# Performance work log

Hardware: AMD Instinct MI355X
Metric: run time of the kernel (lower is better)

## Reference

```python
import jax, jax.numpy as jnp
import numpy as np

EMBED_DIM = 1024
NUM_HEADS = 16
HEAD_DIM = EMBED_DIM // NUM_HEADS
BATCH = 1
SEQ = 4096


def setup_inputs() -> dict:
    key = jax.random.key(0)
    ks = jax.random.split(key, 9)
    s = 1.0 / np.sqrt(EMBED_DIM)
    inp = {
        "x": jax.random.normal(ks[0], (BATCH, SEQ, EMBED_DIM), dtype=jnp.float32),
        "Wq": jax.random.uniform(ks[1], (EMBED_DIM, EMBED_DIM), jnp.float32, -s, s),
        "bq": jax.random.uniform(ks[2], (EMBED_DIM,), jnp.float32, -s, s),
        "Wk": jax.random.uniform(ks[3], (EMBED_DIM, EMBED_DIM), jnp.float32, -s, s),
        "bk": jax.random.uniform(ks[4], (EMBED_DIM,), jnp.float32, -s, s),
        "Wv": jax.random.uniform(ks[5], (EMBED_DIM, EMBED_DIM), jnp.float32, -s, s),
        "bv": jax.random.uniform(ks[6], (EMBED_DIM,), jnp.float32, -s, s),
        "Wo": jax.random.uniform(ks[7], (EMBED_DIM, EMBED_DIM), jnp.float32, -s, s),
        "bo": jax.random.uniform(ks[8], (EMBED_DIM,), jnp.float32, -s, s),
    }
    return inp


def _attention(x, Wq, bq, Wk, bk, Wv, bv, Wo, bo):
    B, S, E = x.shape
    # project and split heads: [B, H, S, D]
    def split_heads(t):
        return t.reshape(B, S, NUM_HEADS, HEAD_DIM).transpose(0, 2, 1, 3)
    q = split_heads(x @ Wq + bq)
    k = split_heads(x @ Wk + bk)
    v = split_heads(x @ Wv + bv)
    scale = 1.0 / np.sqrt(HEAD_DIM).astype(np.float32)
    # scores: [B, H, S, S] (torch code materializes these per query chunk;
    # math is identical computed in one shot)
    scores = jnp.einsum("bhqd,bhkd->bhqk", q, k) * scale
    attn = jax.nn.softmax(scores, axis=-1)  # dropout p=0 -> identity
    out = jnp.einsum("bhqk,bhkd->bhqd", attn, v)
    out = out.transpose(0, 2, 1, 3).reshape(B, S, E)
    return out @ Wo + bo


def reference(x, Wq, bq, Wk, bk, Wv, bv, Wo, bo):
    return _attention(x, Wq, bq, Wk, bk, Wv, bv, Wo, bo)
```

## Files before the change

### kernel.cpp

```cpp
#include <hip/hip_runtime.h>
#include <stdint.h>

typedef __bf16 bf16;
typedef __bf16 bf16x8 __attribute__((ext_vector_type(8)));
typedef float f32x4 __attribute__((ext_vector_type(4)));

#define EMB 1024
#define SEQ 4096
#define NH 16
#define HD 64

__device__ __forceinline__ void glds16(const void* g, void* l) {
    __builtin_amdgcn_global_load_lds(
        (const __attribute__((address_space(1))) uint32_t*)(uintptr_t)g,
        (__attribute__((address_space(3))) uint32_t*)(uintptr_t)l,
        16, 0, 0);
}

__device__ __forceinline__ void transpose_tile(const float* in, bf16* out,
                                               int R, int C, int rbase, int cbase,
                                               bf16* tile ) {
    const int t = threadIdx.x;
#pragma unroll
    for (int p = 0; p < 2; ++p) {
        int idx = t + p * 256;
        int r = idx >> 3;
        int seg = idx & 7;
        const float* src = in + (size_t)(rbase + r) * C + cbase + seg * 8;
        f32x4 a = *(const f32x4*)src;
        f32x4 b = *(const f32x4*)(src + 4);
#pragma unroll
        for (int i = 0; i < 4; ++i) {
            tile[r * 81 + seg * 8 + i]     = (bf16)a[i];
            tile[r * 81 + seg * 8 + 4 + i] = (bf16)b[i];
        }
    }
    __syncthreads();
#pragma unroll
    for (int p = 0; p < 2; ++p) {
        int idx = t + p * 256;
        int r = idx >> 3;
        int seg = idx & 7;
        bf16x8 v;
#pragma unroll
        for (int i = 0; i < 8; ++i) v[i] = tile[(seg * 8 + i) * 81 + r];
        *(bf16x8*)(out + (size_t)(cbase + r) * R + rbase + seg * 8) = v;
    }
}

__global__ __launch_bounds__(256) void prep_k(const float* __restrict__ W0,
                                              const float* __restrict__ W1,
                                              const float* __restrict__ W2,
                                              bf16* __restrict__ o0,
                                              bf16* __restrict__ o1,
                                              bf16* __restrict__ o2,
                                              const float* __restrict__ x,
                                              bf16* __restrict__ xb) {
    __shared__ bf16 tile[64 * 81];
    if (blockIdx.z < 3) {
        const float* in = blockIdx.z == 0 ? W0 : (blockIdx.z == 1 ? W1 : W2);
        bf16* out = blockIdx.z == 0 ? o0 : (blockIdx.z == 1 ? o1 : o2);
        transpose_tile(in, out, EMB, EMB, blockIdx.y * 64, blockIdx.x * 64, tile);
    } else {
        size_t linear = blockIdx.y * 16 + blockIdx.x;
#pragma unroll
        for (int i = 0; i < 4; ++i) {
            size_t base = linear * 16384 + (size_t)i * 4096 + threadIdx.x * 16;
#pragma unroll
            for (int h = 0; h < 2; ++h) {
                f32x4 a = *(const f32x4*)(x + base + h * 8);
                f32x4 b = *(const f32x4*)(x + base + h * 8 + 4);
                bf16x8 v;
#pragma unroll
                for (int j = 0; j < 4; ++j) { v[j] = (bf16)a[j]; v[4 + j] = (bf16)b[j]; }
                *(bf16x8*)(xb + base + h * 8) = v;
            }
        }
    }
}

__global__ __launch_bounds__(256) void transpose_k(const float* __restrict__ in,
                                                   bf16* __restrict__ out,
                                                   int R, int C) {
    __shared__ bf16 tile[64 * 81];
    transpose_tile(in, out, R, C, blockIdx.y * 64, blockIdx.x * 64, tile);
}

template<bool A_BF16, bool FUSED>
__global__ __launch_bounds__(256, 3) void gemm_m97(
    const void* __restrict__ A,
    const bf16* __restrict__ Wt0, const bf16* __restrict__ Wt1,
    const bf16* __restrict__ Wt2,
    const float* __restrict__ b0, const float* __restrict__ b1,
    const float* __restrict__ b2,
    void* __restrict__ out0, void* __restrict__ out1,
    bf16* __restrict__ outVt) {
    constexpr int SMEM_BYTES = A_BF16 ? (FUSED ? 18432 : 16384) : 24576;
    __shared__ __align__(16) uint8_t smem[SMEM_BYTES];
    float* aF = (float*)smem;
    bf16*  aB = (bf16*)smem;
    bf16*  bL = (bf16*)(smem + (A_BF16 ? 8192 : 16384));

    const int t = threadIdx.x;
    const int lane = t & 63;
    const int wave = t >> 6;
    const int l15 = lane & 15;
    const int quad = lane >> 4;
    const int wrow = (wave >> 1) * 64;
    const int wcol = (wave & 1) * 64;
    const int nb = blockIdx.x;
    const int which = FUSED ? (nb >> 3) : 0;
    const int ncol = (FUSED ? (nb & 7) : nb) * 128;
    const int mblock = blockIdx.y * 128;

    const bf16* Wt = FUSED ? (which == 0 ? Wt0 : (which == 1 ? Wt1 : Wt2)) : Wt0;
    const float* bias = FUSED ? (which == 0 ? b0 : (which == 1 ? b1 : b2)) : b0;

    float bv[4];
#pragma unroll
    for (int nt = 0; nt < 4; ++nt) bv[nt] = bias[ncol + wcol + nt * 16 + l15];

    f32x4 acc[4][4];
#pragma unroll
    for (int mt = 0; mt < 4; ++mt)
#pragma unroll
        for (int nt = 0; nt < 4; ++nt) acc[mt][nt] = (f32x4){0.f, 0.f, 0.f, 0.f};

    const int a4row = lane >> 3, a4seg = lane & 7;
    const int b2row = lane >> 2, b2seg = lane & 3;

    for (int k0 = 0; k0 < EMB; k0 += 32) {
        __syncthreads();
        if constexpr (!A_BF16) {
#pragma unroll
            for (int i = 0; i < 4; ++i) {
                int row = i * 32 + wave * 8 + a4row;
                int sg = a4seg ^ (row & 7);
                glds16((const float*)A + (size_t)(mblock + row) * EMB + k0 + sg * 4,
                       smem + i * 4096 + wave * 1024);
            }
        } else {
#pragma unroll
            for (int i = 0; i < 2; ++i) {
                int row = i * 64 + wave * 16 + b2row;
                int sg = b2seg ^ ((row >> 1) & 3);
                glds16((const bf16*)A + (size_t)(mblock + row) * EMB + k0 + sg * 8,
                       smem + i * 4096 + wave * 1024);
            }
        }
#pragma unroll
        for (int i = 0; i < 2; ++i) {
            int row = i * 64 + wave * 16 + b2row;
            int sg = b2seg ^ ((row >> 1) & 3);
            glds16(Wt + (size_t)(ncol + row) * EMB + k0 + sg * 8,
                   (uint8_t*)bL + i * 4096 + wave * 1024);
        }
        __syncthreads();

        bf16x8 af[4], bfr[4];
#pragma unroll
        for (int mt = 0; mt < 4; ++mt) {
            int rl = wrow + mt * 16 + l15;
            if constexpr (!A_BF16) {
                f32x4 lo = *(const f32x4*)(aF + rl * 32 + ((2 * quad)     ^ (rl & 7)) * 4);
                f32x4 hi = *(const f32x4*)(aF + rl * 32 + ((2 * quad + 1) ^ (rl & 7)) * 4);
#pragma unroll
                for (int j = 0; j < 4; ++j) {
                    af[mt][j]     = (bf16)lo[j];
                    af[mt][4 + j] = (bf16)hi[j];
                }
            } else {
                af[mt] = *(const bf16x8*)(aB + rl * 32 + (quad ^ ((rl >> 1) & 3)) * 8);
            }
        }
#pragma unroll
        for (int nt = 0; nt < 4; ++nt) {
            int rl = wcol + nt * 16 + l15;
            bfr[nt] = *(const bf16x8*)(bL + rl * 32 + (quad ^ ((rl >> 1) & 3)) * 8);
        }
#pragma unroll
        for (int mt = 0; mt < 4; ++mt)
#pragma unroll
            for (int nt = 0; nt < 4; ++nt)
                acc[mt][nt] = __builtin_amdgcn_mfma_f32_16x16x32_bf16(
                    af[mt], bfr[nt], acc[mt][nt], 0, 0, 0);
    }

    if (!FUSED || which < 2) {
        void* outp = FUSED ? (which == 0 ? out0 : out1) : out0;
#pragma unroll
        for (int mt = 0; mt < 4; ++mt)
#pragma unroll
            for (int nt = 0; nt < 4; ++nt)
#pragma unroll
                for (int r = 0; r < 4; ++r) {
                    size_t row = mblock + wrow + mt * 16 + quad * 4 + r;
                    size_t col = ncol + wcol + nt * 16 + l15;
                    float v = acc[mt][nt][r] + bv[nt];
                    if constexpr (FUSED) ((bf16*)outp)[row * EMB + col] = (bf16)v;
                    else                 ((float*)outp)[row * EMB + col] = v;
                }
    } else if constexpr (FUSED) {
        __syncthreads();
        bf16* tr = (bf16*)smem + wave * 2304;
#pragma unroll
        for (int ch = 0; ch < 2; ++ch) {
#pragma unroll
            for (int mt = 0; mt < 4; ++mt)
#pragma unroll
                for (int ntl = 0; ntl < 2; ++ntl)
#pragma unroll
                    for (int r = 0; r < 4; ++r) {
                        int d_local = ntl * 16 + l15;
                        int s_local = mt * 16 + quad * 4 + r;
                        int nt = 2 * ch + ntl;
                        tr[d_local * 72 + s_local] = (bf16)(acc[mt][nt][r] + bv[nt]);
                    }
            int d2 = lane & 31, h2 = lane >> 5;
#pragma unroll
            for (int j = 0; j < 4; ++j) {
                bf16x8 v = *(const bf16x8*)(tr + d2 * 72 + h2 * 32 + j * 8);
                *(bf16x8*)(outVt + (size_t)(ncol + wcol + ch * 32 + d2) * SEQ +
                           mblock + wrow + h2 * 32 + j * 8) = v;
            }
        }
    }
}

__global__ __launch_bounds__(256, 2) void attn_k(bf16* __restrict__ QO,
                                                 const bf16* __restrict__ Km,
                                                 const bf16* __restrict__ Vt,
                                                 const float* __restrict__ Wo,
                                                 bf16* __restrict__ wt_o) {
    __shared__ bf16 k_lds[2][64 * 64];
    __shared__ bf16 v_lds[2][64 * 64];
    __shared__ bf16 p_lds[4][2][16][72];

    if (blockIdx.y == NH) {
        bf16* tile = &k_lds[0][0];
#pragma unroll 1
        for (int i = 0; i < 8; ++i) {
            int tid = blockIdx.x * 8 + i;
            int ty = tid >> 4, tx = tid & 15;
            transpose_tile(Wo, wt_o, EMB, EMB, ty * 64, tx * 64, tile);
            __syncthreads();
        }
        return;
    }

    const int t = threadIdx.x;
    const int lane = t & 63;
    const int wave = t >> 6;
    const int l15 = lane & 15;
    const int quad = lane >> 4;
    const int sw = l15 & 7;
    const int h = blockIdx.y;
    const int qbase = blockIdx.x * 128 + wave * 32;
    const float QSCALE = 0.125f * 1.4426950408889634f;

    const int srow = wave * 16 + (lane >> 3);
    const int ssg  = lane & 7;

    bf16x8 qf[2][2];
#pragma unroll
    for (int qt = 0; qt < 2; ++qt)
#pragma unroll
        for (int kk = 0; kk < 2; ++kk) {
            bf16x8 raw = *(const bf16x8*)(QO + (size_t)(qbase + qt * 16 + l15) * EMB +
                                          h * HD + kk * 32 + quad * 8);
#pragma unroll
            for (int j = 0; j < 8; ++j) qf[qt][kk][j] = (bf16)((float)raw[j] * QSCALE);
        }

    f32x4 o_acc[2][4];
#pragma unroll
    for (int qt = 0; qt < 2; ++qt)
#pragma unroll
        for (int c = 0; c < 4; ++c) o_acc[qt][c] = (f32x4){0.f, 0.f, 0.f, 0.f};
    float l_run[2][4] = {{0.f, 0.f, 0.f, 0.f}, {0.f, 0.f, 0.f, 0.f}};

#define STAGE(buf, kbv)                                                               \
    do {                                                                              \
        _Pragma("unroll")                                                             \
        for (int i = 0; i < 2; ++i) {                                                 \
            int rr = srow + i * 8;                                                    \
            int sg = ssg ^ (rr & 7);                                                  \
            glds16(Km + (size_t)((kbv) + rr) * EMB + h * HD + sg * 8,                 \
                   &k_lds[buf][(wave * 16 + i * 8) * 64]);                            \
            glds16(Vt + (size_t)(h * HD + rr) * SEQ + (kbv) + sg * 8,                 \
                   &v_lds[buf][(wave * 16 + i * 8) * 64]);                            \
        }                                                                             \
    } while (0)

#define COMPUTE(buf)                                                                  \
    do {                                                                              \
        f32x4 s[2][4];                                                                \
        _Pragma("unroll")                                                             \
        for (int c = 0; c < 4; ++c) {                                                 \
            int row = c * 16 + l15;                                                   \
            bf16x8 k0 = *(const bf16x8*)&k_lds[buf][row * 64 + ((quad)     ^ sw) * 8];\
            bf16x8 k1 = *(const bf16x8*)&k_lds[buf][row * 64 + ((4 + quad) ^ sw) * 8];\
            _Pragma("unroll")                                                         \
            for (int qt = 0; qt < 2; ++qt) {                                          \
                f32x4 z = (f32x4){0.f, 0.f, 0.f, 0.f};                                \
                z = __builtin_amdgcn_mfma_f32_16x16x32_bf16(qf[qt][0], k0, z, 0, 0, 0);\
                s[qt][c] = __builtin_amdgcn_mfma_f32_16x16x32_bf16(qf[qt][1], k1, z, 0, 0, 0);\
            }                                                                         \
        }                                                                             \
        _Pragma("unroll")                                                             \
        for (int qt = 0; qt < 2; ++qt)                                                \
            _Pragma("unroll")                                                         \
            for (int r = 0; r < 4; ++r)                                               \
                _Pragma("unroll")                                                     \
                for (int c = 0; c < 4; ++c) {                                         \
                    float p = __builtin_amdgcn_exp2f(s[qt][c][r]);                    \
                    l_run[qt][r] += p;                                                \
                    p_lds[wave][qt][quad * 4 + r][c * 16 + l15] = (bf16)p;            \
                }                                                                     \
        bf16x8 pf[2][2];                                                              \
        _Pragma("unroll")                                                             \
        for (int qt = 0; qt < 2; ++qt)                                                \
            _Pragma("unroll")                                                         \
            for (int tt = 0; tt < 2; ++tt)                                            \
                pf[qt][tt] = *(const bf16x8*)&p_lds[wave][qt][l15][tt * 32 + quad * 8];\
        _Pragma("unroll")                                                             \
        for (int c = 0; c < 4; ++c) {                                                 \
            int row = c * 16 + l15;                                                   \
            bf16x8 v0 = *(const bf16x8*)&v_lds[buf][row * 64 + ((quad)     ^ sw) * 8];\
            bf16x8 v1 = *(const bf16x8*)&v_lds[buf][row * 64 + ((4 + quad) ^ sw) * 8];\
            _Pragma("unroll")                                                         \
            for (int qt = 0; qt < 2; ++qt) {                                          \
                o_acc[qt][c] = __builtin_amdgcn_mfma_f32_16x16x32_bf16(               \
                    pf[qt][0], v0, o_acc[qt][c], 0, 0, 0);                            \
                o_acc[qt][c] = __builtin_amdgcn_mfma_f32_16x16x32_bf16(               \
                    pf[qt][1], v1, o_acc[qt][c], 0, 0, 0);                            \
            }                                                                         \
        }                                                                             \
    } while (0)

    STAGE(0, 0);
    for (int kb = 0; kb < SEQ; kb += 128) {
        __syncthreads();
        STAGE(1, kb + 64);
        COMPUTE(0);
        __syncthreads();
        if (kb + 128 < SEQ) STAGE(0, kb + 128);
        COMPUTE(1);
    }
#undef STAGE
#undef COMPUTE

#pragma unroll
    for (int qt = 0; qt < 2; ++qt)
#pragma unroll
        for (int r = 0; r < 4; ++r) {
            float l = l_run[qt][r];
#pragma unroll
            for (int off = 1; off < 16; off <<= 1) l += __shfl_xor(l, off);
            float inv = 1.0f / l;
#pragma unroll
            for (int c = 0; c < 4; ++c)
                QO[(size_t)(qbase + qt * 16 + quad * 4 + r) * EMB + h * HD + c * 16 + l15] =
                    (bf16)(o_acc[qt][c][r] * inv);
        }
}

extern "C" void kernel_launch(void* const* d_in, const int* in_sizes, int n_in,
                              void* d_out, int out_size, void* d_ws, size_t ws_size,
                              hipStream_t stream) {
    const float* x  = (const float*)d_in[0];
    const float* Wq = (const float*)d_in[1];
    const float* bq = (const float*)d_in[2];
    const float* Wk = (const float*)d_in[3];
    const float* bk = (const float*)d_in[4];
    const float* Wv = (const float*)d_in[5];
    const float* bv = (const float*)d_in[6];
    const float* Wo = (const float*)d_in[7];
    const float* bo = (const float*)d_in[8];

    const size_t MAT = (size_t)SEQ * EMB;
    const size_t WMT = (size_t)EMB * EMB;

    bf16* o16   = (bf16*)d_out;
    bf16* Wt_q  = o16;
    bf16* Wt_k  = o16 + WMT;
    bf16* Wt_v  = o16 + 2 * WMT;
    bf16* Vtb   = o16 + 3 * WMT;

    bf16* wsb   = (bf16*)d_ws;
    bf16* QOb   = wsb;
    bf16* Kb    = wsb + MAT;
    bf16* xb    = wsb + 2 * MAT;

    dim3 blk(256);
    dim3 gP(16, 16, 4);
    dim3 gF(24, SEQ / 128);
    dim3 gO(EMB / 128, SEQ / 128);

    if (ws_size >= 3 * MAT * sizeof(bf16)) {
        prep_k<<<gP, blk, 0, stream>>>(Wq, Wk, Wv, Wt_q, Wt_k, Wt_v, x, xb);

        gemm_m97<true, true><<<gF, blk, 0, stream>>>(
            xb, Wt_q, Wt_k, Wt_v, bq, bk, bv, QOb, Kb, Vtb);

        dim3 gA(SEQ / 128, NH + 1);
        attn_k<<<gA, blk, 0, stream>>>(QOb, Kb, Vtb, Wo, xb);

        gemm_m97<true, false><<<gO, blk, 0, stream>>>(
            QOb, xb, nullptr, nullptr, bo, nullptr, nullptr, d_out, nullptr, nullptr);
    } else {
        bf16* Wt_o = wsb + MAT;
        dim3 gTW(EMB / 64, EMB / 64);
        transpose_k<<<gTW, blk, 0, stream>>>(Wq, Wt_q, EMB, EMB);
        transpose_k<<<gTW, blk, 0, stream>>>(Wk, Wt_k, EMB, EMB);
        transpose_k<<<gTW, blk, 0, stream>>>(Wv, Wt_v, EMB, EMB);
        gemm_m97<false, true><<<gF, blk, 0, stream>>>(
            x, Wt_q, Wt_k, Wt_v, bq, bk, bv, QOb, Kb, Vtb);
        dim3 gA(SEQ / 128, NH);
        attn_k<<<gA, blk, 0, stream>>>(QOb, Kb, Vtb, nullptr, nullptr);
        transpose_k<<<gTW, blk, 0, stream>>>(Wo, Wt_o, EMB, EMB);
        gemm_m97<true, false><<<gO, blk, 0, stream>>>(
            QOb, Wt_o, nullptr, nullptr, bo, nullptr, nullptr, d_out, nullptr, nullptr);
    }
}
```

Before: 243.1 us.

## Split attention block into 8 waves of 16 query rows each

The attention kernel now launches 512 threads per block, with each of 8 waves owning 16 query rows instead of 4 waves owning 32. K/V staging is spread over all 8 waves, and the Wo transpose path is templated for 512 threads. The aim is more waves in flight to hide LDS and exp latency, with lower per-wave register pressure. The cost is that each K/V tile loaded into LDS is reused by only one query tile per wave, so there is less MFMA work per LDS read, and barriers now synchronise more waves.

```diff
diff --git a/kernel.cpp b/kernel.cpp
--- a/kernel.cpp
+++ b/kernel.cpp
@@ -17,13 +17,15 @@
         16, 0, 0);
 }
 
+template<int NT>
 __device__ __forceinline__ void transpose_tile(const float* in, bf16* out,
                                                int R, int C, int rbase, int cbase,
                                                bf16* tile ) {
     const int t = threadIdx.x;
-#pragma unroll
-    for (int p = 0; p < 2; ++p) {
-        int idx = t + p * 256;
+    constexpr int PASSES = 512 / NT;
+#pragma unroll
+    for (int p = 0; p < PASSES; ++p) {
+        int idx = t + p * NT;
         int r = idx >> 3;
         int seg = idx & 7;
         const float* src = in + (size_t)(rbase + r) * C + cbase + seg * 8;
@@ -37,8 +39,8 @@
     }
     __syncthreads();
 #pragma unroll
-    for (int p = 0; p < 2; ++p) {
-        int idx = t + p * 256;
+    for (int p = 0; p < PASSES; ++p) {
+        int idx = t + p * NT;
         int r = idx >> 3;
         int seg = idx & 7;
         bf16x8 v;
@@ -60,7 +62,7 @@
     if (blockIdx.z < 3) {
         const float* in = blockIdx.z == 0 ? W0 : (blockIdx.z == 1 ? W1 : W2);
         bf16* out = blockIdx.z == 0 ? o0 : (blockIdx.z == 1 ? o1 : o2);
-        transpose_tile(in, out, EMB, EMB, blockIdx.y * 64, blockIdx.x * 64, tile);
+        transpose_tile<256>(in, out, EMB, EMB, blockIdx.y * 64, blockIdx.x * 64, tile);
     } else {
         size_t linear = blockIdx.y * 16 + blockIdx.x;
 #pragma unroll
@@ -83,7 +85,7 @@
                                                    bf16* __restrict__ out,
                                                    int R, int C) {
     __shared__ bf16 tile[64 * 81];
-    transpose_tile(in, out, R, C, blockIdx.y * 64, blockIdx.x * 64, tile);
+    transpose_tile<256>(in, out, R, C, blockIdx.y * 64, blockIdx.x * 64, tile);
 }
 
 template<bool A_BF16, bool FUSED>
@@ -227,14 +229,14 @@
     }
 }
 
-__global__ __launch_bounds__(256, 2) void attn_k(bf16* __restrict__ QO,
+__global__ __launch_bounds__(512, 4) void attn_k(bf16* __restrict__ QO,
                                                  const bf16* __restrict__ Km,
                                                  const bf16* __restrict__ Vt,
                                                  const float* __restrict__ Wo,
                                                  bf16* __restrict__ wt_o) {
     __shared__ bf16 k_lds[2][64 * 64];
     __shared__ bf16 v_lds[2][64 * 64];
-    __shared__ bf16 p_lds[4][2][16][72];
+    __shared__ bf16 p_lds[8][16][72];
 
     if (blockIdx.y == NH) {
         bf16* tile = &k_lds[0][0];
@@ -242,7 +244,7 @@
         for (int i = 0; i < 8; ++i) {
             int tid = blockIdx.x * 8 + i;
             int ty = tid >> 4, tx = tid & 15;
-            transpose_tile(Wo, wt_o, EMB, EMB, ty * 64, tx * 64, tile);
+            transpose_tile<512>(Wo, wt_o, EMB, EMB, ty * 64, tx * 64, tile);
             __syncthreads();
         }
         return;
@@ -255,86 +257,69 @@
     const int quad = lane >> 4;
     const int sw = l15 & 7;
     const int h = blockIdx.y;
-    const int qbase = blockIdx.x * 128 + wave * 32;
+    const int qrow = blockIdx.x * 128 + wave * 16;
     const float QSCALE = 0.125f * 1.4426950408889634f;
 
-    const int srow = wave * 16 + (lane >> 3);
+    const int srow8 = lane >> 3;
     const int ssg  = lane & 7;
 
-    bf16x8 qf[2][2];
-#pragma unroll
-    for (int qt = 0; qt < 2; ++qt)
-#pragma unroll
-        for (int kk = 0; kk < 2; ++kk) {
-            bf16x8 raw = *(const bf16x8*)(QO + (size_t)(qbase + qt * 16 + l15) * EMB +
-                                          h * HD + kk * 32 + quad * 8);
-#pragma unroll
-            for (int j = 0; j < 8; ++j) qf[qt][kk][j] = (bf16)((float)raw[j] * QSCALE);
-        }
-
-    f32x4 o_acc[2][4];
-#pragma unroll
-    for (int qt = 0; qt < 2; ++qt)
-#pragma unroll
-        for (int c = 0; c < 4; ++c) o_acc[qt][c] = (f32x4){0.f, 0.f, 0.f, 0.f};
-    float l_run[2][4] = {{0.f, 0.f, 0.f, 0.f}, {0.f, 0.f, 0.f, 0.f}};
+    bf16x8 qf[2];
+#pragma unroll
+    for (int kk = 0; kk < 2; ++kk) {
+        bf16x8 raw = *(const bf16x8*)(QO + (size_t)(qrow + l15) * EMB +
+                                      h * HD + kk * 32 + quad * 8);
+#pragma unroll
+        for (int j = 0; j < 8; ++j) qf[kk][j] = (bf16)((float)raw[j] * QSCALE);
+    }
+
+    f32x4 o_acc[4];
+#pragma unroll
+    for (int c = 0; c < 4; ++c) o_acc[c] = (f32x4){0.f, 0.f, 0.f, 0.f};
+    float l_run[4] = {0.f, 0.f, 0.f, 0.f};
 
 #define STAGE(buf, kbv)                                                               \
     do {                                                                              \
-        _Pragma("unroll")                                                             \
-        for (int i = 0; i < 2; ++i) {                                                 \
-            int rr = srow + i * 8;                                                    \
-            int sg = ssg ^ (rr & 7);                                                  \
-            glds16(Km + (size_t)((kbv) + rr) * EMB + h * HD + sg * 8,                 \
-                   &k_lds[buf][(wave * 16 + i * 8) * 64]);                            \
-            glds16(Vt + (size_t)(h * HD + rr) * SEQ + (kbv) + sg * 8,                 \
-                   &v_lds[buf][(wave * 16 + i * 8) * 64]);                            \
-        }                                                                             \
+        int rr = wave * 8 + srow8;                                                    \
+        int sg = ssg ^ (rr & 7);                                                      \
+        glds16(Km + (size_t)((kbv) + rr) * EMB + h * HD + sg * 8,                     \
+               &k_lds[buf][(wave * 8) * 64]);                                         \
+        glds16(Vt + (size_t)(h * HD + rr) * SEQ + (kbv) + sg * 8,                     \
+               &v_lds[buf][(wave * 8) * 64]);                                         \
     } while (0)
 
 #define COMPUTE(buf)                                                                  \
     do {                                                                              \
-        f32x4 s[2][4];                                                                \
+        f32x4 s[4];                                                                   \
         _Pragma("unroll")                                                             \
         for (int c = 0; c < 4; ++c) {                                                 \
             int row = c * 16 + l15;                                                   \
             bf16x8 k0 = *(const bf16x8*)&k_lds[buf][row * 64 + ((quad)     ^ sw) * 8];\
             bf16x8 k1 = *(const bf16x8*)&k_lds[buf][row * 64 + ((4 + quad) ^ sw) * 8];\
-            _Pragma("unroll")                                                         \
-            for (int qt = 0; qt < 2; ++qt) {                                          \
-                f32x4 z = (f32x4){0.f, 0.f, 0.f, 0.f};                                \
-                z = __builtin_amdgcn_mfma_f32_16x16x32_bf16(qf[qt][0], k0, z, 0, 0, 0);\
-                s[qt][c] = __builtin_amdgcn_mfma_f32_16x16x32_bf16(qf[qt][1], k1, z, 0, 0, 0);\
-            }                                                                         \
+            f32x4 z = (f32x4){0.f, 0.f, 0.f, 0.f};                                    \
+            z = __builtin_amdgcn_mfma_f32_16x16x32_bf16(qf[0], k0, z, 0, 0, 0);       \
+            s[c] = __builtin_amdgcn_mfma_f32_16x16x32_bf16(qf[1], k1, z, 0, 0, 0);    \
         }                                                                             \
         _Pragma("unroll")                                                             \
-        for (int qt = 0; qt < 2; ++qt)                                                \
+        for (int r = 0; r < 4; ++r)                                                   \
             _Pragma("unroll")                                                         \
-            for (int r = 0; r < 4; ++r)                                               \
-                _Pragma("unroll")                                                     \
-                for (int c = 0; c < 4; ++c) {                                         \
-                    float p = __builtin_amdgcn_exp2f(s[qt][c][r]);                    \
-                    l_run[qt][r] += p;                                                \
-                    p_lds[wave][qt][quad * 4 + r][c * 16 + l15] = (bf16)p;            \
-                }                                                                     \
-        bf16x8 pf[2][2];                                                              \
+            for (int c = 0; c < 4; ++c) {                                             \
+                float p = __builtin_amdgcn_exp2f(s[c][r]);                            \
+                l_run[r] += p;                                                        \
+                p_lds[wave][quad * 4 + r][c * 16 + l15] = (bf16)p;                    \
+            }                                                                         \
+        bf16x8 pf[2];                                                                 \
         _Pragma("unroll")                                                             \
-        for (int qt = 0; qt < 2; ++qt)                                                \
-            _Pragma("unroll")                                                         \
-            for (int tt = 0; tt < 2; ++tt)                                            \
-                pf[qt][tt] = *(const bf16x8*)&p_lds[wave][qt][l15][tt * 32 + quad * 8];\
+        for (int tt = 0; tt < 2; ++tt)                                                \
+            pf[tt] = *(const bf16x8*)&p_lds[wave][l15][tt * 32 + quad * 8];           \
         _Pragma("unroll")                                                             \
         for (int c = 0; c < 4; ++c) {                                                 \
             int row = c * 16 + l15;                                                   \
             bf16x8 v0 = *(const bf16x8*)&v_lds[buf][row * 64 + ((quad)     ^ sw) * 8];\
             bf16x8 v1 = *(const bf16x8*)&v_lds[buf][row * 64 + ((4 + quad) ^ sw) * 8];\
-            _Pragma("unroll")                                                         \
-            for (int qt = 0; qt < 2; ++qt) {                                          \
-                o_acc[qt][c] = __builtin_amdgcn_mfma_f32_16x16x32_bf16(               \
-                    pf[qt][0], v0, o_acc[qt][c], 0, 0, 0);                            \
-                o_acc[qt][c] = __builtin_amdgcn_mfma_f32_16x16x32_bf16(               \
-                    pf[qt][1], v1, o_acc[qt][c], 0, 0, 0);                            \
-            }                                                                         \
+            o_acc[c] = __builtin_amdgcn_mfma_f32_16x16x32_bf16(                       \
+                pf[0], v0, o_acc[c], 0, 0, 0);                                        \
+            o_acc[c] = __builtin_amdgcn_mfma_f32_16x16x32_bf16(                       \
+                pf[1], v1, o_acc[c], 0, 0, 0);                                        \
         }                                                                             \
     } while (0)
 
@@ -351,18 +336,16 @@
 #undef COMPUTE
 
 #pragma unroll
-    for (int qt = 0; qt < 2; ++qt)
-#pragma unroll
-        for (int r = 0; r < 4; ++r) {
-            float l = l_run[qt][r];
-#pragma unroll
-            for (int off = 1; off < 16; off <<= 1) l += __shfl_xor(l, off);
-            float inv = 1.0f / l;
-#pragma unroll
-            for (int c = 0; c < 4; ++c)
-                QO[(size_t)(qbase + qt * 16 + quad * 4 + r) * EMB + h * HD + c * 16 + l15] =
-                    (bf16)(o_acc[qt][c][r] * inv);
-        }
+    for (int r = 0; r < 4; ++r) {
+        float l = l_run[r];
+#pragma unroll
+        for (int off = 1; off < 16; off <<= 1) l += __shfl_xor(l, off);
+        float inv = 1.0f / l;
+#pragma unroll
+        for (int c = 0; c < 4; ++c)
+            QO[(size_t)(qrow + quad * 4 + r) * EMB + h * HD + c * 16 + l15] =
+                (bf16)(o_acc[c][r] * inv);
+    }
 }
 
 extern "C" void kernel_launch(void* const* d_in, const int* in_sizes, int n_in,
@@ -393,6 +376,7 @@
     bf16* xb    = wsb + 2 * MAT;
 
     dim3 blk(256);
+    dim3 blkA(512);
     dim3 gP(16, 16, 4);
     dim3 gF(24, SEQ / 128);
     dim3 gO(EMB / 128, SEQ / 128);
@@ -404,7 +388,7 @@
             xb, Wt_q, Wt_k, Wt_v, bq, bk, bv, QOb, Kb, Vtb);
 
         dim3 gA(SEQ / 128, NH + 1);
-        attn_k<<<gA, blk, 0, stream>>>(QOb, Kb, Vtb, Wo, xb);
+        attn_k<<<gA, blkA, 0, stream>>>(QOb, Kb, Vtb, Wo, xb);
 
         gemm_m97<true, false><<<gO, blk, 0, stream>>>(
             QOb, xb, nullptr, nullptr, bo, nullptr, nullptr, d_out, nullptr, nullptr);
@@ -417,7 +401,7 @@
         gemm_m97<false, true><<<gF, blk, 0, stream>>>(
             x, Wt_q, Wt_k, Wt_v, bq, bk, bv, QOb, Kb, Vtb);
         dim3 gA(SEQ / 128, NH);
-        attn_k<<<gA, blk, 0, stream>>>(QOb, Kb, Vtb, nullptr, nullptr);
+        attn_k<<<gA, blkA, 0, stream>>>(QOb, Kb, Vtb, nullptr, nullptr);
         transpose_k<<<gTW, blk, 0, stream>>>(Wo, Wt_o, EMB, EMB);
         gemm_m97<true, false><<<gO, blk, 0, stream>>>(
             QOb, Wt_o, nullptr, nullptr, bo, nullptr, nullptr, d_out, nullptr, nullptr);
```

New measurement: 243.3 us. About the same (+0.1%).

## Swap QK^T MFMA operands and redistribute P via lane shuffles instead of LDS

Applied to the files above, without the earlier changes.

Computes S transposed by swapping MFMA operands, so each lane holds four consecutive key columns for one query row. The probabilities are packed to bf16 pairs and rearranged into the A-operand layout for the PV MFMA with xor shuffles, removing the per-wave LDS round trip for P. The row-sum reduction becomes a per-lane accumulation with fewer shuffles. This trades LDS stores and loads for many cross-lane shuffles and selects, which could raise instruction count or register pressure.

```diff
diff --git a/kernel.cpp b/kernel.cpp
--- a/kernel.cpp
+++ b/kernel.cpp
@@ -2,6 +2,7 @@
 #include <stdint.h>
 
 typedef __bf16 bf16;
+typedef __bf16 bf16x2 __attribute__((ext_vector_type(2)));
 typedef __bf16 bf16x8 __attribute__((ext_vector_type(8)));
 typedef float f32x4 __attribute__((ext_vector_type(4)));
 
@@ -17,13 +18,21 @@
         16, 0, 0);
 }
 
+union PU { bf16x2 h; uint32_t u; };
+__device__ __forceinline__ uint32_t pack_bf16(float a, float b) {
+    PU p; p.h = (bf16x2){(bf16)a, (bf16)b}; return p.u;
+}
+union FU { bf16x8 v; uint32_t u[4]; };
+
+template<int NT>
 __device__ __forceinline__ void transpose_tile(const float* in, bf16* out,
                                                int R, int C, int rbase, int cbase,
                                                bf16* tile ) {
     const int t = threadIdx.x;
-#pragma unroll
-    for (int p = 0; p < 2; ++p) {
-        int idx = t + p * 256;
+    constexpr int PASSES = 512 / NT;
+#pragma unroll
+    for (int p = 0; p < PASSES; ++p) {
+        int idx = t + p * NT;
         int r = idx >> 3;
         int seg = idx & 7;
         const float* src = in + (size_t)(rbase + r) * C + cbase + seg * 8;
@@ -37,8 +46,8 @@
     }
     __syncthreads();
 #pragma unroll
-    for (int p = 0; p < 2; ++p) {
-        int idx = t + p * 256;
+    for (int p = 0; p < PASSES; ++p) {
+        int idx = t + p * NT;
         int r = idx >> 3;
         int seg = idx & 7;
         bf16x8 v;
@@ -60,7 +69,7 @@
     if (blockIdx.z < 3) {
         const float* in = blockIdx.z == 0 ? W0 : (blockIdx.z == 1 ? W1 : W2);
         bf16* out = blockIdx.z == 0 ? o0 : (blockIdx.z == 1 ? o1 : o2);
-        transpose_tile(in, out, EMB, EMB, blockIdx.y * 64, blockIdx.x * 64, tile);
+        transpose_tile<256>(in, out, EMB, EMB, blockIdx.y * 64, blockIdx.x * 64, tile);
     } else {
         size_t linear = blockIdx.y * 16 + blockIdx.x;
 #pragma unroll
@@ -83,7 +92,7 @@
                                                    bf16* __restrict__ out,
                                                    int R, int C) {
     __shared__ bf16 tile[64 * 81];
-    transpose_tile(in, out, R, C, blockIdx.y * 64, blockIdx.x * 64, tile);
+    transpose_tile<256>(in, out, R, C, blockIdx.y * 64, blockIdx.x * 64, tile);
 }
 
 template<bool A_BF16, bool FUSED>
@@ -234,7 +243,6 @@
                                                  bf16* __restrict__ wt_o) {
     __shared__ bf16 k_lds[2][64 * 64];
     __shared__ bf16 v_lds[2][64 * 64];
-    __shared__ bf16 p_lds[4][2][16][72];
 
     if (blockIdx.y == NH) {
         bf16* tile = &k_lds[0][0];
@@ -242,7 +250,7 @@
         for (int i = 0; i < 8; ++i) {
             int tid = blockIdx.x * 8 + i;
             int ty = tid >> 4, tx = tid & 15;
-            transpose_tile(Wo, wt_o, EMB, EMB, ty * 64, tx * 64, tile);
+            transpose_tile<256>(Wo, wt_o, EMB, EMB, ty * 64, tx * 64, tile);
             __syncthreads();
         }
         return;
@@ -261,6 +269,10 @@
     const int srow = wave * 16 + (lane >> 3);
     const int ssg  = lane & 7;
 
+    const bool qodd = (quad & 1) != 0;
+    const bool qup  = quad >= 2;
+    const bool qown = (quad == 0) || (quad == 3);
+
     bf16x8 qf[2][2];
 #pragma unroll
     for (int qt = 0; qt < 2; ++qt)
@@ -277,7 +289,7 @@
     for (int qt = 0; qt < 2; ++qt)
 #pragma unroll
         for (int c = 0; c < 4; ++c) o_acc[qt][c] = (f32x4){0.f, 0.f, 0.f, 0.f};
-    float l_run[2][4] = {{0.f, 0.f, 0.f, 0.f}, {0.f, 0.f, 0.f, 0.f}};
+    float l_run[2] = {0.f, 0.f};
 
 #define STAGE(buf, kbv)                                                               \
     do {                                                                              \
@@ -303,26 +315,48 @@
             _Pragma("unroll")                                                         \
             for (int qt = 0; qt < 2; ++qt) {                                          \
                 f32x4 z = (f32x4){0.f, 0.f, 0.f, 0.f};                                \
-                z = __builtin_amdgcn_mfma_f32_16x16x32_bf16(qf[qt][0], k0, z, 0, 0, 0);\
-                s[qt][c] = __builtin_amdgcn_mfma_f32_16x16x32_bf16(qf[qt][1], k1, z, 0, 0, 0);\
+                z = __builtin_amdgcn_mfma_f32_16x16x32_bf16(k0, qf[qt][0], z, 0, 0, 0);\
+                s[qt][c] = __builtin_amdgcn_mfma_f32_16x16x32_bf16(k1, qf[qt][1], z, 0, 0, 0);\
             }                                                                         \
         }                                                                             \
+        uint32_t plo[2][4], phi[2][4];                                                \
         _Pragma("unroll")                                                             \
         for (int qt = 0; qt < 2; ++qt)                                                \
             _Pragma("unroll")                                                         \
-            for (int r = 0; r < 4; ++r)                                               \
-                _Pragma("unroll")                                                     \
-                for (int c = 0; c < 4; ++c) {                                         \
-                    float p = __builtin_amdgcn_exp2f(s[qt][c][r]);                    \
-                    l_run[qt][r] += p;                                                \
-                    p_lds[wave][qt][quad * 4 + r][c * 16 + l15] = (bf16)p;            \
-                }                                                                     \
-        bf16x8 pf[2][2];                                                              \
+            for (int c = 0; c < 4; ++c) {                                             \
+                float p0 = __builtin_amdgcn_exp2f(s[qt][c][0]);                       \
+                float p1 = __builtin_amdgcn_exp2f(s[qt][c][1]);                       \
+                float p2 = __builtin_amdgcn_exp2f(s[qt][c][2]);                       \
+                float p3 = __builtin_amdgcn_exp2f(s[qt][c][3]);                       \
+                l_run[qt] += (p0 + p1) + (p2 + p3);                                   \
+                plo[qt][c] = pack_bf16(p0, p1);                                       \
+                phi[qt][c] = pack_bf16(p2, p3);                                       \
+            }                                                                         \
+        FU F[2][2];                                                                   \
         _Pragma("unroll")                                                             \
-        for (int qt = 0; qt < 2; ++qt)                                                \
+        for (int qt = 0; qt < 2; ++qt) {                                              \
+            uint32_t a0[4], a1[4], a2[4], a3[4];                                      \
             _Pragma("unroll")                                                         \
-            for (int tt = 0; tt < 2; ++tt)                                            \
-                pf[qt][tt] = *(const bf16x8*)&p_lds[wave][qt][l15][tt * 32 + quad * 8];\
+            for (int c = 0; c < 4; ++c) {                                             \
+                uint32_t ol = (uint32_t)__shfl_xor((int)plo[qt][c], 16);              \
+                uint32_t oh = (uint32_t)__shfl_xor((int)phi[qt][c], 16);              \
+                a0[c] = qodd ? ol : plo[qt][c];                                       \
+                a1[c] = qodd ? oh : phi[qt][c];                                       \
+                a2[c] = qodd ? plo[qt][c] : ol;                                       \
+                a3[c] = qodd ? phi[qt][c] : oh;                                       \
+            }                                                                         \
+            _Pragma("unroll")                                                         \
+            for (int tt = 0; tt < 2; ++tt) {                                          \
+                uint32_t r0 = (uint32_t)__shfl_xor((int)(qup ? a0[2*tt] : a0[2*tt+1]), 32); \
+                uint32_t r1 = (uint32_t)__shfl_xor((int)(qup ? a1[2*tt] : a1[2*tt+1]), 32); \
+                uint32_t r2 = (uint32_t)__shfl_xor((int)(qup ? a2[2*tt] : a2[2*tt+1]), 32); \
+                uint32_t r3 = (uint32_t)__shfl_xor((int)(qup ? a3[2*tt] : a3[2*tt+1]), 32); \
+                F[qt][tt].u[0] = qown ? (qup ? a0[2*tt+1] : a0[2*tt]) : r0;           \
+                F[qt][tt].u[1] = qown ? (qup ? a1[2*tt+1] : a1[2*tt]) : r1;           \
+                F[qt][tt].u[2] = qown ? (qup ? a2[2*tt+1] : a2[2*tt]) : r2;           \
+                F[qt][tt].u[3] = qown ? (qup ? a3[2*tt+1] : a3[2*tt]) : r3;           \
+            }                                                                         \
+        }                                                                             \
         _Pragma("unroll")                                                             \
         for (int c = 0; c < 4; ++c) {                                                 \
             int row = c * 16 + l15;                                                   \
@@ -331,9 +365,9 @@
             _Pragma("unroll")                                                         \
             for (int qt = 0; qt < 2; ++qt) {                                          \
                 o_acc[qt][c] = __builtin_amdgcn_mfma_f32_16x16x32_bf16(               \
-                    pf[qt][0], v0, o_acc[qt][c], 0, 0, 0);                            \
+                    F[qt][0].v, v0, o_acc[qt][c], 0, 0, 0);                           \
                 o_acc[qt][c] = __builtin_amdgcn_mfma_f32_16x16x32_bf16(               \
-                    pf[qt][1], v1, o_acc[qt][c], 0, 0, 0);                            \
+                    F[qt][1].v, v1, o_acc[qt][c], 0, 0, 0);                           \
             }                                                                         \
         }                                                                             \
     } while (0)
@@ -351,18 +385,20 @@
 #undef COMPUTE
 
 #pragma unroll
-    for (int qt = 0; qt < 2; ++qt)
+    for (int qt = 0; qt < 2; ++qt) {
+        float l = l_run[qt];
+        l += __shfl_xor(l, 16);
+        l += __shfl_xor(l, 32);
+        float inv = 1.0f / l;
 #pragma unroll
         for (int r = 0; r < 4; ++r) {
-            float l = l_run[qt][r];
-#pragma unroll
-            for (int off = 1; off < 16; off <<= 1) l += __shfl_xor(l, off);
-            float inv = 1.0f / l;
+            float invr = __shfl(inv, quad * 4 + r);
 #pragma unroll
             for (int c = 0; c < 4; ++c)
                 QO[(size_t)(qbase + qt * 16 + quad * 4 + r) * EMB + h * HD + c * 16 + l15] =
-                    (bf16)(o_acc[qt][c][r] * inv);
-        }
+                    (bf16)(o_acc[qt][c][r] * invr);
+        }
+    }
 }
 
 extern "C" void kernel_launch(void* const* d_in, const int* in_sizes, int n_in,
```

Result: slower. 270.3 us (+11.2%).
